# Kernel optimization log

Hardware: AMD Instinct MI355X
Metric: run time of the kernel (lower is better)

The kernel has to match this reference:

```python
import jax, jax.numpy as jnp
import numpy as np

B, N, D, H = 4, 2048, 256, 8
HD = D // H  # head_dim = 32


def setup_inputs() -> dict:
    key = jax.random.key(0)
    ks = jax.random.split(key, 9)
    s = 1.0 / np.sqrt(D)
    return {
        "x": jax.random.normal(ks[0], (B, N, D), dtype=jnp.float32),
        "Wq": jax.random.normal(ks[1], (D, D), dtype=jnp.float32) * s,
        "bq": jnp.zeros((D,), dtype=jnp.float32),
        "Wk": jax.random.normal(ks[2], (D, D), dtype=jnp.float32) * s,
        "bk": jnp.zeros((D,), dtype=jnp.float32),
        "Wv": jax.random.normal(ks[3], (D, D), dtype=jnp.float32) * s,
        "bv": jnp.zeros((D,), dtype=jnp.float32),
        "Wo": jax.random.normal(ks[4], (D, D), dtype=jnp.float32) * s,
        "bo": jnp.zeros((D,), dtype=jnp.float32),
    }


def reference(x, Wq, bq, Wk, bk, Wv, bv, Wo, bo):
    # x: (B, N, D). Weights follow torch Linear convention: y = x @ W.T + b
    def split_heads(t):  # (B, N, D) -> (B, H, N, HD)
        return t.reshape(B, N, H, HD).transpose(0, 2, 1, 3)

    Q = split_heads(x @ Wq.T + bq)
    K = split_heads(x @ Wk.T + bk)
    V = split_heads(x @ Wv.T + bv)

    scores = jnp.einsum('bhqd,bhkd->bhqk', Q, K) / np.sqrt(HD)
    attention = jax.nn.softmax(scores, axis=-1)  # explicit (B,H,N,N) weights
    # dropout is identity in eval mode
    attended = jnp.einsum('bhqk,bhkd->bhqd', attention, V)
    attended = attended.transpose(0, 2, 1, 3).reshape(B, N, D)
    output = attended @ Wo.T + bo
    return output
```

## Files before the change

### kernel.cpp

```cpp
#include <hip/hip_runtime.h>
#include <math.h>

#define D_MODEL 256
#define NSEQ    2048
#define BATCH   4
#define NHEAD   8
#define HDIM    32
#define SCL2E   0.25506372769861746f

typedef __attribute__((ext_vector_type(8))) short  short8;
typedef __attribute__((ext_vector_type(4))) float  f32x4;
typedef __attribute__((ext_vector_type(4))) unsigned int u32x4;
typedef __attribute__((ext_vector_type(2))) unsigned int u32x2;
typedef unsigned short u16;
typedef unsigned int   u32;

__device__ __forceinline__ u16 f2bf(float f) {
    union { float f; u32 u; } v; v.f = f;
    u32 r = v.u + 0x7FFFu + ((v.u >> 16) & 1u);
    return (u16)(r >> 16);
}
__device__ __forceinline__ u32 cvtpk(float lo, float hi) {
    u32 r; asm("v_cvt_pk_bf16_f32 %0, %1, %2" : "=v"(r) : "v"(lo), "v"(hi));
    return r;
}
__device__ __forceinline__ float fexp2(float x) {
    float r; asm("v_exp_f32 %0, %1" : "=v"(r) : "v"(x)); return r;
}
__device__ __forceinline__ void gload16(const u16* gsrc, u16* ldst) {
    __builtin_amdgcn_global_load_lds(
        (const __attribute__((address_space(1))) unsigned int*)gsrc,
        (__attribute__((address_space(3))) unsigned int*)ldst, 16, 0, 0);
}

__global__ __launch_bounds__(256) void cvt_w_kernel(
    const float* __restrict__ w0, const float* __restrict__ w1,
    const float* __restrict__ w2, const float* __restrict__ w3,
    u16* __restrict__ Wall)
{
    int i = blockIdx.x * 256 + threadIdx.x;
    int which = i >> 13;
    const float* src = which == 0 ? w0 : which == 1 ? w1 : which == 2 ? w2 : w3;
    u16* dst = Wall + (size_t)which * 65536;
    size_t off = i & 8191;
    const float4* s4 = (const float4*)src;
    float4 a = s4[2 * off], b = s4[2 * off + 1];
    u32x4 o;
    o.x = (u32)f2bf(a.x) | ((u32)f2bf(a.y) << 16);
    o.y = (u32)f2bf(a.z) | ((u32)f2bf(a.w) << 16);
    o.z = (u32)f2bf(b.x) | ((u32)f2bf(b.y) << 16);
    o.w = (u32)f2bf(b.z) | ((u32)f2bf(b.w) << 16);
    *(u32x4*)(dst + off * 8) = o;
}

__global__ __launch_bounds__(256) void gemm_qkv_kernel(
    const float* __restrict__ x, const u16* __restrict__ Wall,
    const float* __restrict__ bq, const float* __restrict__ bk,
    const float* __restrict__ bv,
    u16* __restrict__ Qo, u16* __restrict__ Ko, u16* __restrict__ Vto)
{
    __shared__ u16 Xs[64][264];
    __shared__ u16 Lw[4][2560];

    const int z  = blockIdx.y;
    const int m0 = blockIdx.x * 64;
    const u16* W = Wall + (size_t)z * 65536;
    const float* bias = z == 0 ? bq : (z == 1 ? bk : bv);

    const int tid = threadIdx.x, wid = tid >> 6, l = tid & 63;
    const int lq = l & 15, g = l >> 4;

    {
        const int row = tid >> 2, qt = (tid & 3) * 64;
        const float* src = x + (size_t)(m0 + row) * 256 + qt;
        u16* dst = &Xs[row][qt];
        #pragma unroll
        for (int i = 0; i < 8; ++i) {
            float4 a = *(const float4*)(src + i * 8);
            float4 c = *(const float4*)(src + i * 8 + 4);
            union { u32 u[4]; short8 s8; } pk;
            pk.u[0] = cvtpk(a.x, a.y); pk.u[1] = cvtpk(a.z, a.w);
            pk.u[2] = cvtpk(c.x, c.y); pk.u[3] = cvtpk(c.z, c.w);
            *(short8*)(dst + i * 8) = pk.s8;
        }
    }
    __syncthreads();

    const int nwb = wid * 64;
    f32x4 acc[4][4];
    #pragma unroll
    for (int s = 0; s < 4; ++s)
        #pragma unroll
        for (int ns = 0; ns < 4; ++ns) acc[s][ns] = (f32x4){0.f, 0.f, 0.f, 0.f};

    #pragma unroll
    for (int kk = 0; kk < 8; ++kk) {
        short8 af[4];
        #pragma unroll
        for (int s = 0; s < 4; ++s)
            af[s] = *(const short8*)&Xs[s * 16 + lq][kk * 32 + g * 8];
        #pragma unroll
        for (int ns = 0; ns < 4; ++ns) {
            short8 wf = *(const short8*)(W + (size_t)(nwb + ns * 16 + lq) * 256 + kk * 32 + g * 8);
            #pragma unroll
            for (int s = 0; s < 4; ++s)
                acc[s][ns] = __builtin_amdgcn_mfma_f32_16x16x32_bf16(af[s], wf, acc[s][ns], 0, 0, 0);
        }
    }

    const int b = m0 >> 11, seq0 = m0 & 2047;
    u16* Lp = &Lw[wid][0];

    if (z < 2) {
        const float sc = (z == 0) ? SCL2E : 1.0f;
        u16* out = (z == 0) ? Qo : Ko;
        #pragma unroll
        for (int hp = 0; hp < 2; ++hp) {
            #pragma unroll
            for (int ns2 = 0; ns2 < 2; ++ns2) {
                const int ns = hp * 2 + ns2;
                const float bb = bias[nwb + ns * 16 + lq];
                #pragma unroll
                for (int s = 0; s < 4; ++s)
                    #pragma unroll
                    for (int r = 0; r < 4; ++r)
                        Lp[(s * 16 + g * 4 + r) * 40 + ns2 * 16 + lq] =
                            f2bf((acc[s][ns][r] + bb) * sc);
            }
            const int h = wid * 2 + hp;
            u16* op = out + ((size_t)(b * 8 + h) * 2048 + seq0 + l) * 32;
            #pragma unroll
            for (int c = 0; c < 4; ++c)
                *(short8*)(op + c * 8) = *(const short8*)&Lp[l * 40 + c * 8];
        }
    } else {
        #pragma unroll
        for (int hp = 0; hp < 2; ++hp) {
            #pragma unroll
            for (int ns2 = 0; ns2 < 2; ++ns2) {
                const int ns = hp * 2 + ns2;
                const float bb = bias[nwb + ns * 16 + lq];
                #pragma unroll
                for (int s = 0; s < 4; ++s)
                    #pragma unroll
                    for (int r = 0; r < 4; ++r)
                        Lp[(ns2 * 16 + lq) * 72 + s * 16 + g * 4 + r] =
                            f2bf(acc[s][ns][r] + bb);
            }
            const int h = wid * 2 + hp;
            #pragma unroll
            for (int i = 0; i < 4; ++i) {
                const int dd = (l >> 3) + i * 8, ck = l & 7;
                short8 v = *(const short8*)&Lp[dd * 72 + ck * 8];
                *(short8*)(Vto + ((size_t)(b * 8 + h) * 32 + dd) * 2048 + seq0 + ck * 8) = v;
            }
        }
    }
}

__global__ __launch_bounds__(256) void gemm_out_kernel(
    const u16* __restrict__ A, const u16* __restrict__ W,
    const float* __restrict__ bias, float* __restrict__ Cout)
{
    const int tid = threadIdx.x, wid = tid >> 6, l = tid & 63;
    const int lq = l & 15, g = l >> 4;
    const int m0 = blockIdx.y * 64;
    const int nw = blockIdx.x * 128 + wid * 32;

    f32x4 acc[4][2];
    #pragma unroll
    for (int s = 0; s < 4; ++s)
        #pragma unroll
        for (int ns = 0; ns < 2; ++ns) acc[s][ns] = (f32x4){0.f, 0.f, 0.f, 0.f};

    #pragma unroll
    for (int kk = 0; kk < 8; ++kk) {
        short8 af[4];
        #pragma unroll
        for (int s = 0; s < 4; ++s)
            af[s] = *(const short8*)(A + (size_t)(m0 + s * 16 + lq) * 256 + kk * 32 + g * 8);
        #pragma unroll
        for (int ns = 0; ns < 2; ++ns) {
            short8 wf = *(const short8*)(W + (size_t)(nw + ns * 16 + lq) * 256 + kk * 32 + g * 8);
            #pragma unroll
            for (int s = 0; s < 4; ++s)
                acc[s][ns] = __builtin_amdgcn_mfma_f32_16x16x32_bf16(af[s], wf, acc[s][ns], 0, 0, 0);
        }
    }

    #pragma unroll
    for (int ns = 0; ns < 2; ++ns) {
        const int n = nw + ns * 16 + lq;
        const float bb = bias[n];
        #pragma unroll
        for (int s = 0; s < 4; ++s)
            #pragma unroll
            for (int r = 0; r < 4; ++r)
                Cout[(size_t)(m0 + s * 16 + g * 4 + r) * 256 + n] = acc[s][ns][r] + bb;
    }
}

__global__ __launch_bounds__(128, 2) void attn_kernel(
    const u16* __restrict__ Q, const u16* __restrict__ K,
    const u16* __restrict__ Vt, u16* __restrict__ Oa)
{
    __shared__ u16 Kbuf[3][64 * 32];
    __shared__ u16 Vbuf[3][32 * 64];
    __shared__ u16 Pl[2][2][16 * 72];

    const int tid = threadIdx.x, wid = tid >> 6, l = tid & 63;
    const int lq = l & 15, g = l >> 4;
    const int bh = blockIdx.y;
    const int q0 = blockIdx.x * 64 + wid * 32;

    const u16* Qb = Q  + ((size_t)bh * 2048 + q0) * 32;
    const u16* Kb = K  + (size_t)bh * 2048 * 32;
    const u16* Vb = Vt + (size_t)bh * 32 * 2048;

    const int krow = tid >> 2;
    const int ksl  = (tid & 3) ^ ((krow >> 1) & 3);
    const u16* KsrcA = Kb + krow * 32 + ksl * 8;
    const int vrow = tid >> 3;
    const int vsl  = (tid & 7) ^ (vrow & 7);
    const u16* VsrcA = Vb + (size_t)vrow * 2048 + vsl * 8;

    const int kswz = (g ^ ((lq >> 1) & 3)) * 8;
    const int vswz = lq & 7;

    const short8 qfa = *(const short8*)(Qb + lq * 32 + g * 8);
    const short8 qfb = *(const short8*)(Qb + (16 + lq) * 32 + g * 8);

    f32x4 oa0 = (f32x4){0,0,0,0}, oa1 = oa0, ob0 = oa0, ob1 = oa0;
    float la = 0.f, lb = 0.f;

    u16* PA = &Pl[wid][0][0];
    u16* PB = &Pl[wid][1][0];

    auto stage = [&](int kt, int buf) {
        gload16(KsrcA + kt * 2048,        &Kbuf[buf][tid * 8]);
        gload16(KsrcA + kt * 2048 + 1024, &Kbuf[buf][tid * 8 + 1024]);
        gload16(VsrcA + kt * 64,             &Vbuf[buf][tid * 8]);
        gload16(VsrcA + kt * 64 + 16 * 2048, &Vbuf[buf][tid * 8 + 1024]);
    };

    stage(0, 0);
    stage(1, 1);

    int cur = 0;
    for (int kt = 0; kt < 32; ++kt) {
        if (kt < 31) asm volatile("s_waitcnt vmcnt(4)" ::: "memory");
        else         asm volatile("s_waitcnt vmcnt(0)" ::: "memory");
        __builtin_amdgcn_s_barrier();

        if (kt + 2 < 32) {
            const int nb = cur + 2 >= 3 ? cur - 1 : cur + 2;
            stage(kt + 2, nb);
        }

        const u16* KB = &Kbuf[cur][0];
        const u16* VB = &Vbuf[cur][0];

        short8 kf[4], vf[2][2];
        #pragma unroll
        for (int s = 0; s < 4; ++s)
            kf[s] = *(const short8*)&KB[(s * 16 + lq) * 32 + kswz];
        #pragma unroll
        for (int hh = 0; hh < 2; ++hh)
            #pragma unroll
            for (int kc = 0; kc < 2; ++kc)
                vf[hh][kc] = *(const short8*)&VB[(hh * 16 + lq) * 64 + (((kc * 4 + g) ^ vswz) * 8)];

        const f32x4 zz = (f32x4){0.f, 0.f, 0.f, 0.f};
        f32x4 sfa[4], sfb[4];
        __builtin_amdgcn_s_setprio(1);
        #pragma unroll
        for (int s = 0; s < 4; ++s)
            sfa[s] = __builtin_amdgcn_mfma_f32_16x16x32_bf16(kf[s], qfa, zz, 0, 0, 0);
        #pragma unroll
        for (int s = 0; s < 4; ++s)
            sfb[s] = __builtin_amdgcn_mfma_f32_16x16x32_bf16(kf[s], qfb, zz, 0, 0, 0);
        __builtin_amdgcn_s_setprio(0);

        #pragma unroll
        for (int s = 0; s < 4; ++s) {
            float p0 = fexp2(sfa[s][0]), p1 = fexp2(sfa[s][1]);
            float p2 = fexp2(sfa[s][2]), p3 = fexp2(sfa[s][3]);
            la += (p0 + p1) + (p2 + p3);
            u32x2 w; w.x = cvtpk(p0, p1); w.y = cvtpk(p2, p3);
            *(u32x2*)&PA[lq * 72 + s * 16 + g * 4] = w;
        }
        #pragma unroll
        for (int s = 0; s < 4; ++s) {
            float p0 = fexp2(sfb[s][0]), p1 = fexp2(sfb[s][1]);
            float p2 = fexp2(sfb[s][2]), p3 = fexp2(sfb[s][3]);
            lb += (p0 + p1) + (p2 + p3);
            u32x2 w; w.x = cvtpk(p0, p1); w.y = cvtpk(p2, p3);
            *(u32x2*)&PB[lq * 72 + s * 16 + g * 4] = w;
        }

        __builtin_amdgcn_s_setprio(1);
        #pragma unroll
        for (int kc = 0; kc < 2; ++kc) {
            short8 pa = *(const short8*)&PA[lq * 72 + kc * 32 + g * 8];
            short8 pb = *(const short8*)&PB[lq * 72 + kc * 32 + g * 8];
            oa0 = __builtin_amdgcn_mfma_f32_16x16x32_bf16(pa, vf[0][kc], oa0, 0, 0, 0);
            oa1 = __builtin_amdgcn_mfma_f32_16x16x32_bf16(pa, vf[1][kc], oa1, 0, 0, 0);
            ob0 = __builtin_amdgcn_mfma_f32_16x16x32_bf16(pb, vf[0][kc], ob0, 0, 0, 0);
            ob1 = __builtin_amdgcn_mfma_f32_16x16x32_bf16(pb, vf[1][kc], ob1, 0, 0, 0);
        }
        __builtin_amdgcn_s_setprio(0);

        cur = cur + 1 >= 3 ? 0 : cur + 1;
    }

    la += __shfl_xor(la, 16); la += __shfl_xor(la, 32);
    lb += __shfl_xor(lb, 16); lb += __shfl_xor(lb, 32);

    const int b = bh >> 3, h = bh & 7;
    #pragma unroll
    for (int r = 0; r < 4; ++r) {
        const float inva = __builtin_amdgcn_rcpf(__shfl(la, g * 4 + r));
        const float invb = __builtin_amdgcn_rcpf(__shfl(lb, g * 4 + r));
        const int seqa = q0 + g * 4 + r, seqb = seqa + 16;
        const size_t ba  = ((size_t)(b * 2048 + seqa)) * 256 + h * 32;
        const size_t bb2 = ((size_t)(b * 2048 + seqb)) * 256 + h * 32;
        Oa[ba + lq]       = f2bf(oa0[r] * inva);
        Oa[ba + 16 + lq]  = f2bf(oa1[r] * inva);
        Oa[bb2 + lq]      = f2bf(ob0[r] * invb);
        Oa[bb2 + 16 + lq] = f2bf(ob1[r] * invb);
    }
}

extern "C" void kernel_launch(void* const* d_in, const int* in_sizes, int n_in,
                              void* d_out, int out_size, void* d_ws, size_t ws_size,
                              hipStream_t stream)
{
    const float* x  = (const float*)d_in[0];
    const float* Wq = (const float*)d_in[1];
    const float* bq = (const float*)d_in[2];
    const float* Wk = (const float*)d_in[3];
    const float* bk = (const float*)d_in[4];
    const float* Wv = (const float*)d_in[5];
    const float* bv = (const float*)d_in[6];
    const float* Wo = (const float*)d_in[7];
    const float* bo = (const float*)d_in[8];
    float* out = (float*)d_out;

    u16* wsp  = (u16*)d_ws;
    u16* Wall = wsp;
    u16* Qh   = Wall + (size_t)4 * 65536;
    u16* Kh   = Qh + (size_t)8192 * 256;
    u16* Vth  = Kh + (size_t)8192 * 256;
    u16* Ab   = Vth + (size_t)8192 * 256;

    cvt_w_kernel<<<128, 256, 0, stream>>>(Wq, Wk, Wv, Wo, Wall);
    gemm_qkv_kernel<<<dim3(128, 3), 256, 0, stream>>>(x, Wall, bq, bk, bv, Qh, Kh, Vth);
    attn_kernel<<<dim3(32, 32), 128, 0, stream>>>(Qh, Kh, Vth, Ab);
    gemm_out_kernel<<<dim3(2, 128), 256, 0, stream>>>(Ab, Wall + (size_t)3 * 65536, bo, out);
}
```

Before: 71.67 us.

## Keep softmax probabilities in registers by permuting K rows; use 4 waves per block

The attention kernel no longer routes the P tile through LDS. K rows are loaded in a permuted order so that the S accumulator layout of each lane directly matches the A-operand layout of the PV MFMA, which lets the bf16 probabilities be packed in registers. Each block now runs 4 waves of 16 queries instead of 2 waves of 32, so each wave computes half as many MFMAs while the K/V staging cost is spread over more threads. This removes LDS writes and reads plus their latency, in exchange for less reuse of K/V fragments per wave and more waves per block.

New measurement: 64.23 us. 10.4% less time.

```diff
diff --git a/kernel.cpp b/kernel.cpp
--- a/kernel.cpp
+++ b/kernel.cpp
@@ -11,7 +11,6 @@
 typedef __attribute__((ext_vector_type(8))) short  short8;
 typedef __attribute__((ext_vector_type(4))) float  f32x4;
 typedef __attribute__((ext_vector_type(4))) unsigned int u32x4;
-typedef __attribute__((ext_vector_type(2))) unsigned int u32x2;
 typedef unsigned short u16;
 typedef unsigned int   u32;
 
@@ -200,47 +199,40 @@
     }
 }
 
-__global__ __launch_bounds__(128, 2) void attn_kernel(
+__global__ __launch_bounds__(256, 4) void attn_kernel(
     const u16* __restrict__ Q, const u16* __restrict__ K,
     const u16* __restrict__ Vt, u16* __restrict__ Oa)
 {
     __shared__ u16 Kbuf[3][64 * 32];
     __shared__ u16 Vbuf[3][32 * 64];
-    __shared__ u16 Pl[2][2][16 * 72];
 
     const int tid = threadIdx.x, wid = tid >> 6, l = tid & 63;
     const int lq = l & 15, g = l >> 4;
     const int bh = blockIdx.y;
-    const int q0 = blockIdx.x * 64 + wid * 32;
+    const int q0 = blockIdx.x * 64 + wid * 16;
 
     const u16* Qb = Q  + ((size_t)bh * 2048 + q0) * 32;
     const u16* Kb = K  + (size_t)bh * 2048 * 32;
     const u16* Vb = Vt + (size_t)bh * 32 * 2048;
 
-    const int krow = tid >> 2;
-    const int ksl  = (tid & 3) ^ ((krow >> 1) & 3);
-    const u16* KsrcA = Kb + krow * 32 + ksl * 8;
-    const int vrow = tid >> 3;
-    const int vsl  = (tid & 7) ^ (vrow & 7);
-    const u16* VsrcA = Vb + (size_t)vrow * 2048 + vsl * 8;
+    const int u  = tid >> 2;
+    const int ug = (u & 0x20) | ((u & 0x0C) << 1) | ((u & 0x10) >> 2) | (u & 0x03);
+    const int ksl = (tid & 3) ^ ((u >> 1) & 3);
+    const u16* Ksrc = Kb + ug * 32 + ksl * 8;
+    const int vd = tid >> 3, vsl = (tid & 7) ^ (vd & 7);
+    const u16* Vsrc = Vb + (size_t)vd * 2048 + vsl * 8;
 
     const int kswz = (g ^ ((lq >> 1) & 3)) * 8;
     const int vswz = lq & 7;
 
-    const short8 qfa = *(const short8*)(Qb + lq * 32 + g * 8);
-    const short8 qfb = *(const short8*)(Qb + (16 + lq) * 32 + g * 8);
-
-    f32x4 oa0 = (f32x4){0,0,0,0}, oa1 = oa0, ob0 = oa0, ob1 = oa0;
-    float la = 0.f, lb = 0.f;
-
-    u16* PA = &Pl[wid][0][0];
-    u16* PB = &Pl[wid][1][0];
+    const short8 qf = *(const short8*)(Qb + lq * 32 + g * 8);
+
+    f32x4 o0 = (f32x4){0.f, 0.f, 0.f, 0.f}, o1 = o0;
+    float la = 0.f;
 
     auto stage = [&](int kt, int buf) {
-        gload16(KsrcA + kt * 2048,        &Kbuf[buf][tid * 8]);
-        gload16(KsrcA + kt * 2048 + 1024, &Kbuf[buf][tid * 8 + 1024]);
-        gload16(VsrcA + kt * 64,             &Vbuf[buf][tid * 8]);
-        gload16(VsrcA + kt * 64 + 16 * 2048, &Vbuf[buf][tid * 8 + 1024]);
+        gload16(Ksrc + kt * 2048, &Kbuf[buf][tid * 8]);
+        gload16(Vsrc + kt * 64,   &Vbuf[buf][tid * 8]);
     };
 
     stage(0, 0);
@@ -248,7 +240,7 @@
 
     int cur = 0;
     for (int kt = 0; kt < 32; ++kt) {
-        if (kt < 31) asm volatile("s_waitcnt vmcnt(4)" ::: "memory");
+        if (kt < 31) asm volatile("s_waitcnt vmcnt(2)" ::: "memory");
         else         asm volatile("s_waitcnt vmcnt(0)" ::: "memory");
         __builtin_amdgcn_s_barrier();
 
@@ -271,63 +263,52 @@
                 vf[hh][kc] = *(const short8*)&VB[(hh * 16 + lq) * 64 + (((kc * 4 + g) ^ vswz) * 8)];
 
         const f32x4 zz = (f32x4){0.f, 0.f, 0.f, 0.f};
-        f32x4 sfa[4], sfb[4];
+        f32x4 sf[4];
         __builtin_amdgcn_s_setprio(1);
         #pragma unroll
         for (int s = 0; s < 4; ++s)
-            sfa[s] = __builtin_amdgcn_mfma_f32_16x16x32_bf16(kf[s], qfa, zz, 0, 0, 0);
-        #pragma unroll
-        for (int s = 0; s < 4; ++s)
-            sfb[s] = __builtin_amdgcn_mfma_f32_16x16x32_bf16(kf[s], qfb, zz, 0, 0, 0);
+            sf[s] = __builtin_amdgcn_mfma_f32_16x16x32_bf16(kf[s], qf, zz, 0, 0, 0);
         __builtin_amdgcn_s_setprio(0);
 
-        #pragma unroll
-        for (int s = 0; s < 4; ++s) {
-            float p0 = fexp2(sfa[s][0]), p1 = fexp2(sfa[s][1]);
-            float p2 = fexp2(sfa[s][2]), p3 = fexp2(sfa[s][3]);
-            la += (p0 + p1) + (p2 + p3);
-            u32x2 w; w.x = cvtpk(p0, p1); w.y = cvtpk(p2, p3);
-            *(u32x2*)&PA[lq * 72 + s * 16 + g * 4] = w;
-        }
-        #pragma unroll
-        for (int s = 0; s < 4; ++s) {
-            float p0 = fexp2(sfb[s][0]), p1 = fexp2(sfb[s][1]);
-            float p2 = fexp2(sfb[s][2]), p3 = fexp2(sfb[s][3]);
-            lb += (p0 + p1) + (p2 + p3);
-            u32x2 w; w.x = cvtpk(p0, p1); w.y = cvtpk(p2, p3);
-            *(u32x2*)&PB[lq * 72 + s * 16 + g * 4] = w;
-        }
+        float p00 = fexp2(sf[0][0]), p01 = fexp2(sf[0][1]);
+        float p02 = fexp2(sf[0][2]), p03 = fexp2(sf[0][3]);
+        float p10 = fexp2(sf[1][0]), p11 = fexp2(sf[1][1]);
+        float p12 = fexp2(sf[1][2]), p13 = fexp2(sf[1][3]);
+        float p20 = fexp2(sf[2][0]), p21 = fexp2(sf[2][1]);
+        float p22 = fexp2(sf[2][2]), p23 = fexp2(sf[2][3]);
+        float p30 = fexp2(sf[3][0]), p31 = fexp2(sf[3][1]);
+        float p32 = fexp2(sf[3][2]), p33 = fexp2(sf[3][3]);
+
+        la += ((p00 + p01) + (p02 + p03)) + ((p10 + p11) + (p12 + p13))
+            + ((p20 + p21) + (p22 + p23)) + ((p30 + p31) + (p32 + p33));
+
+        union { u32 w[4]; short8 s8; } pa0, pa1;
+        pa0.w[0] = cvtpk(p00, p01); pa0.w[1] = cvtpk(p02, p03);
+        pa0.w[2] = cvtpk(p10, p11); pa0.w[3] = cvtpk(p12, p13);
+        pa1.w[0] = cvtpk(p20, p21); pa1.w[1] = cvtpk(p22, p23);
+        pa1.w[2] = cvtpk(p30, p31); pa1.w[3] = cvtpk(p32, p33);
 
         __builtin_amdgcn_s_setprio(1);
-        #pragma unroll
-        for (int kc = 0; kc < 2; ++kc) {
-            short8 pa = *(const short8*)&PA[lq * 72 + kc * 32 + g * 8];
-            short8 pb = *(const short8*)&PB[lq * 72 + kc * 32 + g * 8];
-            oa0 = __builtin_amdgcn_mfma_f32_16x16x32_bf16(pa, vf[0][kc], oa0, 0, 0, 0);
-            oa1 = __builtin_amdgcn_mfma_f32_16x16x32_bf16(pa, vf[1][kc], oa1, 0, 0, 0);
-            ob0 = __builtin_amdgcn_mfma_f32_16x16x32_bf16(pb, vf[0][kc], ob0, 0, 0, 0);
-            ob1 = __builtin_amdgcn_mfma_f32_16x16x32_bf16(pb, vf[1][kc], ob1, 0, 0, 0);
-        }
+        o0 = __builtin_amdgcn_mfma_f32_16x16x32_bf16(pa0.s8, vf[0][0], o0, 0, 0, 0);
+        o1 = __builtin_amdgcn_mfma_f32_16x16x32_bf16(pa0.s8, vf[1][0], o1, 0, 0, 0);
+        o0 = __builtin_amdgcn_mfma_f32_16x16x32_bf16(pa1.s8, vf[0][1], o0, 0, 0, 0);
+        o1 = __builtin_amdgcn_mfma_f32_16x16x32_bf16(pa1.s8, vf[1][1], o1, 0, 0, 0);
         __builtin_amdgcn_s_setprio(0);
 
         cur = cur + 1 >= 3 ? 0 : cur + 1;
     }
 
-    la += __shfl_xor(la, 16); la += __shfl_xor(la, 32);
-    lb += __shfl_xor(lb, 16); lb += __shfl_xor(lb, 32);
+    la += __shfl_xor(la, 16);
+    la += __shfl_xor(la, 32);
 
     const int b = bh >> 3, h = bh & 7;
     #pragma unroll
     for (int r = 0; r < 4; ++r) {
-        const float inva = __builtin_amdgcn_rcpf(__shfl(la, g * 4 + r));
-        const float invb = __builtin_amdgcn_rcpf(__shfl(lb, g * 4 + r));
-        const int seqa = q0 + g * 4 + r, seqb = seqa + 16;
-        const size_t ba  = ((size_t)(b * 2048 + seqa)) * 256 + h * 32;
-        const size_t bb2 = ((size_t)(b * 2048 + seqb)) * 256 + h * 32;
-        Oa[ba + lq]       = f2bf(oa0[r] * inva);
-        Oa[ba + 16 + lq]  = f2bf(oa1[r] * inva);
-        Oa[bb2 + lq]      = f2bf(ob0[r] * invb);
-        Oa[bb2 + 16 + lq] = f2bf(ob1[r] * invb);
+        const float inv = __builtin_amdgcn_rcpf(__shfl(la, g * 4 + r));
+        const int seq = q0 + g * 4 + r;
+        const size_t ba = ((size_t)(b * 2048 + seq)) * 256 + h * 32;
+        Oa[ba + lq]      = f2bf(o0[r] * inv);
+        Oa[ba + 16 + lq] = f2bf(o1[r] * inv);
     }
 }
 
@@ -355,6 +336,6 @@
 
     cvt_w_kernel<<<128, 256, 0, stream>>>(Wq, Wk, Wv, Wo, Wall);
     gemm_qkv_kernel<<<dim3(128, 3), 256, 0, stream>>>(x, Wall, bq, bk, bv, Qh, Kh, Vth);
-    attn_kernel<<<dim3(32, 32), 128, 0, stream>>>(Qh, Kh, Vth, Ab);
+    attn_kernel<<<dim3(32, 32), 256, 0, stream>>>(Qh, Kh, Vth, Ab);
     gemm_out_kernel<<<dim3(2, 128), 256, 0, stream>>>(Ab, Wall + (size_t)3 * 65536, bo, out);
 }
```
